# Performance work log

Measured on AMD Instinct MI355X. Metric: run time of the kernel, lower is better.

The kernel has to match this reference:

```python
import jax, jax.numpy as jnp
import numpy as np

NUM_CLASSES = 1000
FEAT_DIM = 128
N = 500000
MOMENTUM = 0.9


def setup_inputs() -> dict:
    key = jax.random.key(0)
    k1, k2, k3, k4 = jax.random.split(key, 4)
    cls_ids = jax.random.randint(k1, (N,), 0, NUM_CLASSES, dtype=jnp.int64 if jax.config.jax_enable_x64 else jnp.int32)
    feats = jax.random.normal(k2, (N, FEAT_DIM), dtype=jnp.float32)
    vec = jax.random.normal(k3, (NUM_CLASSES, FEAT_DIM), dtype=jnp.float32)
    cnt = jax.random.randint(k4, (NUM_CLASSES,), 0, 2, dtype=jnp.int64 if jax.config.jax_enable_x64 else jnp.int32)
    return {"cls_ids": cls_ids, "feats": feats, "vec": vec, "cnt": cnt}


def reference(cls_ids, feats, vec, cnt):
    """Fused segment-mean + EMA prototype update (equivalent to EMAPrototypes.update).

    Returns (new_vec [C,D], new_cnt [C]).
    """
    # per-class counts and feature sums via scatter-reduce
    counts = jax.ops.segment_sum(jnp.ones_like(cls_ids, dtype=jnp.float32), cls_ids,
                                 num_segments=NUM_CLASSES)          # [C]
    sums = jax.ops.segment_sum(feats, cls_ids, num_segments=NUM_CLASSES)  # [C, D]
    present = counts > 0                                             # [C]
    mu = sums / jnp.maximum(counts, 1.0)[:, None]                    # [C, D] per-class mean
    # EMA: fresh classes (cnt==0) take mu directly, else momentum blend
    ema = jnp.where((cnt == 0)[:, None], mu, MOMENTUM * vec + (1.0 - MOMENTUM) * mu)
    new_vec = jnp.where(present[:, None], ema, vec)                  # untouched classes keep old vec
    new_cnt = cnt + counts.astype(cnt.dtype)
    return new_vec, new_cnt
```

## Files before the change

### kernel.cpp

```cpp
#include <hip/hip_runtime.h>

#define C_CLASSES 1000
#define FEAT      128
#define MOM       0.9f
#define CAP       1024
#define CHUNK     2048
#define TPB_S     512
#define TPB_G     512
#define NWAVE_G   (TPB_G / 64)

__global__ __launch_bounds__(TPB_S) void class_scatter_kernel(
    const int* __restrict__ ids, int* __restrict__ cursor,
    int* __restrict__ sorted, int N)
{
    __shared__ int hist[C_CLASSES];
    __shared__ int bb[C_CLASSES];
    __shared__ int cur[C_CLASSES];

    const int tid = threadIdx.x;
    for (int c = tid; c < C_CLASSES; c += TPB_S) { hist[c] = 0; cur[c] = 0; }
    __syncthreads();

    const int base = blockIdx.x * CHUNK + tid * 4;
    int myid[4];
    if (base + 4 <= N) {
        const int4 a = *reinterpret_cast<const int4*>(ids + base);
        myid[0] = a.x; myid[1] = a.y; myid[2] = a.z; myid[3] = a.w;
    } else {
#pragma unroll
        for (int j = 0; j < 4; ++j)
            myid[j] = (base + j < N) ? ids[base + j] : -1;
    }
#pragma unroll
    for (int j = 0; j < 4; ++j)
        if ((unsigned)myid[j] < (unsigned)C_CLASSES) atomicAdd(&hist[myid[j]], 1);
    __syncthreads();

    for (int c = tid; c < C_CLASSES; c += TPB_S) {
        const int h = hist[c];
        bb[c] = h ? atomicAdd(&cursor[c], h) : 0;
    }
    __syncthreads();

#pragma unroll
    for (int j = 0; j < 4; ++j) {
        const int c = myid[j];
        if ((unsigned)c < (unsigned)C_CLASSES) {
            const int r   = atomicAdd(&cur[c], 1);
            const int pos = bb[c] + r;
            if (pos < CAP) sorted[c * CAP + pos] = base + j;
        }
    }
}

__global__ __launch_bounds__(TPB_G) void gather_ema_kernel(
    const float* __restrict__ feats, const int* __restrict__ sorted,
    const int* __restrict__ cursor, const float* __restrict__ vec,
    const int* __restrict__ cnt, float* __restrict__ out)
{
    __shared__ float s_red[NWAVE_G][FEAT];

    const int c     = blockIdx.x;
    const int tid   = threadIdx.x;
    const int lane  = tid & 63;
    const int wid   = tid >> 6;
    const int half  = lane >> 5;
    const int col   = lane & 31;

    const int n_raw = cursor[c];
    const int n     = min(n_raw, CAP);
    const int* sc   = sorted + c * CAP;

    const int q  = (n + NWAVE_G - 1) / NWAVE_G;
    const int w0 = wid * q;
    const int w1 = min(w0 + q, n);
    const int m  = (w1 > w0) ? (w1 - w0) : 0;

    float4 acc = make_float4(0.f, 0.f, 0.f, 0.f);
    if (m > 0) {
        const int mlast = m - 1;
        for (int p = 0; p < m; p += 16) {
            int   idx[8];
            float wgt[8];
#pragma unroll
            for (int u = 0; u < 8; ++u) {
                const int pos = p + u * 2 + half;
                idx[u] = sc[w0 + min(pos, mlast)];
                wgt[u] = (pos < m) ? 1.f : 0.f;
            }
#pragma unroll
            for (int u = 0; u < 8; ++u) {
                const float4 v = *reinterpret_cast<const float4*>(
                    feats + (size_t)idx[u] * FEAT + col * 4);
                acc.x += v.x * wgt[u];
                acc.y += v.y * wgt[u];
                acc.z += v.z * wgt[u];
                acc.w += v.w * wgt[u];
            }
        }
    }

    acc.x += __shfl_xor(acc.x, 32);
    acc.y += __shfl_xor(acc.y, 32);
    acc.z += __shfl_xor(acc.z, 32);
    acc.w += __shfl_xor(acc.w, 32);
    if (half == 0)
        *reinterpret_cast<float4*>(&s_red[wid][col * 4]) = acc;
    __syncthreads();

    if (tid < FEAT) {
        float sum = 0.f;
#pragma unroll
        for (int w = 0; w < NWAVE_G; ++w) sum += s_red[w][tid];
        const float old = vec[c * FEAT + tid];
        const int   oc  = cnt[c];
        const float mu  = sum / fmaxf((float)n_raw, 1.f);
        const float ema = (oc == 0) ? mu : (MOM * old + (1.0f - MOM) * mu);
        out[c * FEAT + tid] = (n_raw > 0) ? ema : old;
    }
    if (tid == FEAT)
        out[C_CLASSES * FEAT + c] = (float)(cnt[c] + n_raw);
}

#define G_F     4
#define QCAP_F  768
#define TPB_F   512
#define NWAVE_F (TPB_F / 64)

__global__ __launch_bounds__(TPB_F) void ema_proto_kernel(
    const int* __restrict__ ids, const float* __restrict__ feats,
    const float* __restrict__ vec, const int* __restrict__ cnt,
    float* __restrict__ out, int N)
{
    __shared__ int   qbuf[NWAVE_F][QCAP_F];
    __shared__ float s_acc[NWAVE_F][G_F][FEAT];
    __shared__ float s_n[NWAVE_F][G_F];

    const int tid  = threadIdx.x;
    const int lane = tid & 63;
    const int wid  = tid >> 6;
    const int c0   = blockIdx.x * G_F;
    const unsigned long long lmask_lt = (1ull << lane) - 1ull;

    const int N4    = N >> 2;
    const int iters = (N4 + TPB_F - 1) / TPB_F;
    const int4* ids4 = reinterpret_cast<const int4*>(ids);
    int qn = 0;
    for (int k = 0; k < iters; ++k) {
        const int i4 = tid + k * TPB_F;
        int4 v;
        if (i4 < N4) v = ids4[i4];
        else         v = make_int4(-1, -1, -1, -1);
        const int idv[4] = {v.x, v.y, v.z, v.w};
#pragma unroll
        for (int j = 0; j < 4; ++j) {
            const unsigned g = (unsigned)idv[j] - (unsigned)c0;
            const bool m = (g < G_F);
            const unsigned long long bal = __ballot(m);
            if (bal) {
                if (m) {
                    const int slot = qn + __popcll(bal & lmask_lt);
                    if (slot < QCAP_F)
                        qbuf[wid][slot] = (((i4 << 2) | j) << 2) | (int)g;
                }
                qn += __popcll(bal);
            }
        }
    }
    if (qn > QCAP_F) qn = QCAP_F;

    float2 a[G_F];
    float  n[G_F];
#pragma unroll
    for (int g = 0; g < G_F; ++g) { a[g].x = 0.f; a[g].y = 0.f; n[g] = 0.f; }
    const int qn_pad = (qn + 3) & ~3;
    for (int q = 0; q < qn_pad; q += 4) {
#pragma unroll
        for (int u = 0; u < 4; ++u) {
            const int  qi   = q + u;
            const bool val  = (qi < qn);
            const int  pack = val ? qbuf[wid][qi] : 0;
            const int  row  = pack >> 2;
            const unsigned g = (unsigned)(pack & 3);
            const float w = val ? 1.f : 0.f;
            const float2 fv = *reinterpret_cast<const float2*>(
                feats + (size_t)row * FEAT + lane * 2);
#pragma unroll
            for (int k = 0; k < G_F; ++k) {
                const float wk = (g == (unsigned)k) ? w : 0.f;
                a[k].x += fv.x * wk;
                a[k].y += fv.y * wk;
                n[k]   += wk;
            }
        }
    }

#pragma unroll
    for (int g = 0; g < G_F; ++g)
        *reinterpret_cast<float2*>(&s_acc[wid][g][lane * 2]) = a[g];
    if (lane == 0) {
#pragma unroll
        for (int g = 0; g < G_F; ++g) s_n[wid][g] = n[g];
    }
    __syncthreads();

    {
        const int g = tid >> 7;
        const int d = tid & 127;
        float sum = 0.f, cf = 0.f;
#pragma unroll
        for (int w = 0; w < NWAVE_F; ++w) {
            sum += s_acc[w][g][d];
            cf  += s_n[w][g];
        }
        const int c = c0 + g;
        const float old = vec[c * FEAT + d];
        const int   oc  = cnt[c];
        const float mu  = sum / fmaxf(cf, 1.f);
        const float ema = (oc == 0) ? mu : (MOM * old + (1.0f - MOM) * mu);
        out[c * FEAT + d] = (cf > 0.f) ? ema : old;
        if (d == 0)
            out[C_CLASSES * FEAT + c] = (float)(oc + (int)cf);
    }
}

extern "C" void kernel_launch(void* const* d_in, const int* in_sizes, int n_in,
                              void* d_out, int out_size, void* d_ws, size_t ws_size,
                              hipStream_t stream) {
    const int*   ids   = (const int*)d_in[0];
    const float* feats = (const float*)d_in[1];
    const float* vec   = (const float*)d_in[2];
    const int*   cnt   = (const int*)d_in[3];
    float*       out   = (float*)d_out;
    const int N = in_sizes[0];

    const size_t need = (size_t)(1024 + C_CLASSES * CAP) * sizeof(int);
    if (ws_size >= need) {
        int* cursor = (int*)d_ws;
        int* sorted = cursor + 1024;
        hipMemsetAsync(cursor, 0, 1024 * sizeof(int), stream);
        const int nblk = (N + CHUNK - 1) / CHUNK;
        hipLaunchKernelGGL(class_scatter_kernel, dim3(nblk), dim3(TPB_S), 0, stream,
                           ids, cursor, sorted, N);
        hipLaunchKernelGGL(gather_ema_kernel, dim3(C_CLASSES), dim3(TPB_G), 0, stream,
                           feats, sorted, cursor, vec, cnt, out);
    } else {
        hipLaunchKernelGGL(ema_proto_kernel, dim3(C_CLASSES / G_F), dim3(TPB_F), 0, stream,
                           ids, feats, vec, cnt, out, N);
    }
}
```

Baseline: 59.28 us.

## Fuse memset, scatter and gather into one cooperative kernel with grid syncs

Replaces the memset plus two-kernel sequence with a single cooperative launch of 512 blocks. Grid-wide syncs separate three phases: zeroing the cursors, the class scatter, and the per-class gather/EMA, where each block handles up to two classes. The aim is to remove launch overheads and the inter-kernel gaps. In exchange it adds grid-sync cost and halves gather parallelism to 512 blocks. It relies on the cooperative launch succeeding and falls back to the old path on error. Note that N/CHUNK is about 245 blocks, so blocks beyond that skip the scatter phase.

```diff
diff --git a/kernel.cpp b/kernel.cpp
--- a/kernel.cpp
+++ b/kernel.cpp
@@ -1,15 +1,141 @@
 #include <hip/hip_runtime.h>
+#include <hip/hip_cooperative_groups.h>
+namespace cg = cooperative_groups;
 
 #define C_CLASSES 1000
 #define FEAT      128
 #define MOM       0.9f
 #define CAP       1024
 #define CHUNK     2048
-#define TPB_S     512
-#define TPB_G     512
-#define NWAVE_G   (TPB_G / 64)
-
-__global__ __launch_bounds__(TPB_S) void class_scatter_kernel(
+#define TPB       512
+#define NWAVE     (TPB / 64)
+#define NBLK      512
+
+__global__ __launch_bounds__(TPB) void fused_ema_kernel(
+    const int* __restrict__ ids, const float* __restrict__ feats,
+    const float* __restrict__ vec, const int* __restrict__ cnt,
+    int* cursor, int* sorted, float* __restrict__ out, int N)
+{
+    cg::grid_group grid = cg::this_grid();
+
+    __shared__ int   hist[C_CLASSES];
+    __shared__ int   bb[C_CLASSES];
+    __shared__ int   cur[C_CLASSES];
+    __shared__ float s_red[NWAVE][FEAT];
+
+    const int tid = threadIdx.x;
+    const int bid = blockIdx.x;
+
+    const int gt = bid * TPB + tid;
+    if (gt < C_CLASSES) cursor[gt] = 0;
+    for (int c = tid; c < C_CLASSES; c += TPB) { hist[c] = 0; cur[c] = 0; }
+
+    grid.sync();
+
+    const int base0 = bid * CHUNK;
+    if (base0 < N) {
+        const int base = base0 + tid * 4;
+        int myid[4];
+        if (base + 4 <= N) {
+            const int4 a = *reinterpret_cast<const int4*>(ids + base);
+            myid[0] = a.x; myid[1] = a.y; myid[2] = a.z; myid[3] = a.w;
+        } else {
+#pragma unroll
+            for (int j = 0; j < 4; ++j)
+                myid[j] = (base + j < N) ? ids[base + j] : -1;
+        }
+#pragma unroll
+        for (int j = 0; j < 4; ++j)
+            if ((unsigned)myid[j] < (unsigned)C_CLASSES) atomicAdd(&hist[myid[j]], 1);
+        __syncthreads();
+
+        for (int c = tid; c < C_CLASSES; c += TPB) {
+            const int h = hist[c];
+            bb[c] = h ? atomicAdd(&cursor[c], h) : 0;
+        }
+        __syncthreads();
+
+#pragma unroll
+        for (int j = 0; j < 4; ++j) {
+            const int c = myid[j];
+            if ((unsigned)c < (unsigned)C_CLASSES) {
+                const int r   = atomicAdd(&cur[c], 1);
+                const int pos = bb[c] + r;
+                if (pos < CAP) sorted[c * CAP + pos] = base + j;
+            }
+        }
+    }
+
+    grid.sync();
+
+    const int lane = tid & 63;
+    const int wid  = tid >> 6;
+    const int half = lane >> 5;
+    const int col  = lane & 31;
+
+#pragma unroll
+    for (int cc = 0; cc < 2; ++cc) {
+        const int c = bid + cc * NBLK;
+        if (c >= C_CLASSES) break;
+        __syncthreads();
+
+        const int n_raw = cursor[c];
+        const int n     = min(n_raw, CAP);
+        const int* sc   = sorted + c * CAP;
+
+        const int q  = (n + NWAVE - 1) / NWAVE;
+        const int w0 = wid * q;
+        const int w1 = min(w0 + q, n);
+        const int m  = (w1 > w0) ? (w1 - w0) : 0;
+
+        float4 acc = make_float4(0.f, 0.f, 0.f, 0.f);
+        if (m > 0) {
+            const int mlast = m - 1;
+            for (int p = 0; p < m; p += 16) {
+                int   idx[8];
+                float wgt[8];
+#pragma unroll
+                for (int u = 0; u < 8; ++u) {
+                    const int pos = p + u * 2 + half;
+                    idx[u] = sc[w0 + min(pos, mlast)];
+                    wgt[u] = (pos < m) ? 1.f : 0.f;
+                }
+#pragma unroll
+                for (int u = 0; u < 8; ++u) {
+                    const float4 v = *reinterpret_cast<const float4*>(
+                        feats + (size_t)idx[u] * FEAT + col * 4);
+                    acc.x += v.x * wgt[u];
+                    acc.y += v.y * wgt[u];
+                    acc.z += v.z * wgt[u];
+                    acc.w += v.w * wgt[u];
+                }
+            }
+        }
+
+        acc.x += __shfl_xor(acc.x, 32);
+        acc.y += __shfl_xor(acc.y, 32);
+        acc.z += __shfl_xor(acc.z, 32);
+        acc.w += __shfl_xor(acc.w, 32);
+        if (half == 0)
+            *reinterpret_cast<float4*>(&s_red[wid][col * 4]) = acc;
+        __syncthreads();
+
+        if (tid < FEAT) {
+            float sum = 0.f;
+#pragma unroll
+            for (int w = 0; w < NWAVE; ++w) sum += s_red[w][tid];
+            const float old = vec[c * FEAT + tid];
+            const int   oc  = cnt[c];
+            const float mu  = sum / fmaxf((float)n_raw, 1.f);
+            const float ema = (oc == 0) ? mu : (MOM * old + (1.0f - MOM) * mu);
+            out[c * FEAT + tid] = (n_raw > 0) ? ema : old;
+        }
+        if (tid == FEAT)
+            out[C_CLASSES * FEAT + c] = (float)(cnt[c] + n_raw);
+    }
+}
+
+__global__ __launch_bounds__(TPB) void class_scatter_kernel(
     const int* __restrict__ ids, int* __restrict__ cursor,
     int* __restrict__ sorted, int N)
 {
@@ -18,7 +144,7 @@
     __shared__ int cur[C_CLASSES];
 
     const int tid = threadIdx.x;
-    for (int c = tid; c < C_CLASSES; c += TPB_S) { hist[c] = 0; cur[c] = 0; }
+    for (int c = tid; c < C_CLASSES; c += TPB) { hist[c] = 0; cur[c] = 0; }
     __syncthreads();
 
     const int base = blockIdx.x * CHUNK + tid * 4;
@@ -36,7 +162,7 @@
         if ((unsigned)myid[j] < (unsigned)C_CLASSES) atomicAdd(&hist[myid[j]], 1);
     __syncthreads();
 
-    for (int c = tid; c < C_CLASSES; c += TPB_S) {
+    for (int c = tid; c < C_CLASSES; c += TPB) {
         const int h = hist[c];
         bb[c] = h ? atomicAdd(&cursor[c], h) : 0;
     }
@@ -53,12 +179,12 @@
     }
 }
 
-__global__ __launch_bounds__(TPB_G) void gather_ema_kernel(
+__global__ __launch_bounds__(TPB) void gather_ema_kernel(
     const float* __restrict__ feats, const int* __restrict__ sorted,
     const int* __restrict__ cursor, const float* __restrict__ vec,
     const int* __restrict__ cnt, float* __restrict__ out)
 {
-    __shared__ float s_red[NWAVE_G][FEAT];
+    __shared__ float s_red[NWAVE][FEAT];
 
     const int c     = blockIdx.x;
     const int tid   = threadIdx.x;
@@ -71,7 +197,7 @@
     const int n     = min(n_raw, CAP);
     const int* sc   = sorted + c * CAP;
 
-    const int q  = (n + NWAVE_G - 1) / NWAVE_G;
+    const int q  = (n + NWAVE - 1) / NWAVE;
     const int w0 = wid * q;
     const int w1 = min(w0 + q, n);
     const int m  = (w1 > w0) ? (w1 - w0) : 0;
@@ -111,7 +237,7 @@
     if (tid < FEAT) {
         float sum = 0.f;
 #pragma unroll
-        for (int w = 0; w < NWAVE_G; ++w) sum += s_red[w][tid];
+        for (int w = 0; w < NWAVE; ++w) sum += s_red[w][tid];
         const float old = vec[c * FEAT + tid];
         const int   oc  = cnt[c];
         const float mu  = sum / fmaxf((float)n_raw, 1.f);
@@ -124,17 +250,15 @@
 
 #define G_F     4
 #define QCAP_F  768
-#define TPB_F   512
-#define NWAVE_F (TPB_F / 64)
-
-__global__ __launch_bounds__(TPB_F) void ema_proto_kernel(
+
+__global__ __launch_bounds__(TPB) void ema_proto_kernel(
     const int* __restrict__ ids, const float* __restrict__ feats,
     const float* __restrict__ vec, const int* __restrict__ cnt,
     float* __restrict__ out, int N)
 {
-    __shared__ int   qbuf[NWAVE_F][QCAP_F];
-    __shared__ float s_acc[NWAVE_F][G_F][FEAT];
-    __shared__ float s_n[NWAVE_F][G_F];
+    __shared__ int   qbuf[NWAVE][QCAP_F];
+    __shared__ float s_acc[NWAVE][G_F][FEAT];
+    __shared__ float s_n[NWAVE][G_F];
 
     const int tid  = threadIdx.x;
     const int lane = tid & 63;
@@ -143,11 +267,11 @@
     const unsigned long long lmask_lt = (1ull << lane) - 1ull;
 
     const int N4    = N >> 2;
-    const int iters = (N4 + TPB_F - 1) / TPB_F;
+    const int iters = (N4 + TPB - 1) / TPB;
     const int4* ids4 = reinterpret_cast<const int4*>(ids);
     int qn = 0;
     for (int k = 0; k < iters; ++k) {
-        const int i4 = tid + k * TPB_F;
+        const int i4 = tid + k * TPB;
         int4 v;
         if (i4 < N4) v = ids4[i4];
         else         v = make_int4(-1, -1, -1, -1);
@@ -155,10 +279,10 @@
 #pragma unroll
         for (int j = 0; j < 4; ++j) {
             const unsigned g = (unsigned)idv[j] - (unsigned)c0;
-            const bool m = (g < G_F);
-            const unsigned long long bal = __ballot(m);
+            const bool mm = (g < G_F);
+            const unsigned long long bal = __ballot(mm);
             if (bal) {
-                if (m) {
+                if (mm) {
                     const int slot = qn + __popcll(bal & lmask_lt);
                     if (slot < QCAP_F)
                         qbuf[wid][slot] = (((i4 << 2) | j) << 2) | (int)g;
@@ -209,7 +333,7 @@
         const int d = tid & 127;
         float sum = 0.f, cf = 0.f;
 #pragma unroll
-        for (int w = 0; w < NWAVE_F; ++w) {
+        for (int w = 0; w < NWAVE; ++w) {
             sum += s_acc[w][g][d];
             cf  += s_n[w][g];
         }
@@ -232,20 +356,29 @@
     const float* vec   = (const float*)d_in[2];
     const int*   cnt   = (const int*)d_in[3];
     float*       out   = (float*)d_out;
-    const int N = in_sizes[0];
+    int N = in_sizes[0];
 
     const size_t need = (size_t)(1024 + C_CLASSES * CAP) * sizeof(int);
     if (ws_size >= need) {
         int* cursor = (int*)d_ws;
         int* sorted = cursor + 1024;
-        hipMemsetAsync(cursor, 0, 1024 * sizeof(int), stream);
-        const int nblk = (N + CHUNK - 1) / CHUNK;
-        hipLaunchKernelGGL(class_scatter_kernel, dim3(nblk), dim3(TPB_S), 0, stream,
-                           ids, cursor, sorted, N);
-        hipLaunchKernelGGL(gather_ema_kernel, dim3(C_CLASSES), dim3(TPB_G), 0, stream,
-                           feats, sorted, cursor, vec, cnt, out);
+
+        void* args[] = { (void*)&ids, (void*)&feats, (void*)&vec, (void*)&cnt,
+                         (void*)&cursor, (void*)&sorted, (void*)&out, (void*)&N };
+        hipError_t err = hipLaunchCooperativeKernel(
+            reinterpret_cast<void*>(fused_ema_kernel),
+            dim3(NBLK), dim3(TPB), args, 0, stream);
+
+        if (err != hipSuccess) {
+            hipMemsetAsync(cursor, 0, 1024 * sizeof(int), stream);
+            const int nblk = (N + CHUNK - 1) / CHUNK;
+            hipLaunchKernelGGL(class_scatter_kernel, dim3(nblk), dim3(TPB), 0, stream,
+                               ids, cursor, sorted, N);
+            hipLaunchKernelGGL(gather_ema_kernel, dim3(C_CLASSES), dim3(TPB), 0, stream,
+                               feats, sorted, cursor, vec, cnt, out);
+        }
     } else {
-        hipLaunchKernelGGL(ema_proto_kernel, dim3(C_CLASSES / G_F), dim3(TPB_F), 0, stream,
+        hipLaunchKernelGGL(ema_proto_kernel, dim3(C_CLASSES / G_F), dim3(TPB), 0, stream,
                            ids, feats, vec, cnt, out, N);
     }
 }
```

New measurement: 167.2 us. +182.0%, slower.
